# Optimization experiments

Hardware: AMD Instinct MI355X
Metric: run time of the kernel (lower is better)

Reference implementation:

```python
import jax, jax.numpy as jnp
import numpy as np

TOP_K = 30
NUM_RBF = 16
MAX_REL = 32  # max_relative_feature
LN_EPS = 1e-5


def normalize(x, axis=-1, eps=1e-12):
    n = jnp.linalg.norm(x, axis=axis, keepdims=True)
    return x / jnp.maximum(n, eps)


def gather_nodes(nodes, idx):
    # nodes [B,L,C], idx [B,L,K] -> [B,L,K,C]
    B, L, K = idx.shape
    flat = idx.reshape(B, L * K)
    g = jnp.take_along_axis(nodes, flat[:, :, None], axis=1)
    return g.reshape(B, L, K, -1)


def gather_edges(edges, idx):
    # edges [B,L,L,C], idx [B,L,K] -> [B,L,K,C]
    return jnp.take_along_axis(edges, idx[..., None], axis=2)


def _dist(Xca, mask, eps=1e-6):
    mask_2D = mask[:, None, :] * mask[:, :, None]            # [B,L,L]
    dX = Xca[:, None, :, :] - Xca[:, :, None, :]             # [B,L,L,3]
    D = mask_2D * jnp.sqrt(jnp.sum(dX ** 2, -1) + eps)
    D_max = jnp.max(D, -1, keepdims=True)
    D_adjust = D + (1.0 - mask_2D) * D_max
    k = min(TOP_K, Xca.shape[1])
    neg_vals, E_idx = jax.lax.top_k(-D_adjust, k)            # smallest-k
    D_neighbors = -neg_vals
    mask_neighbors = gather_edges(mask_2D[..., None], E_idx)
    return D_neighbors, E_idx, mask_neighbors


def _rbf(D):
    D_mu = jnp.linspace(2.0, 22.0, NUM_RBF)                  # [R]
    D_sigma = (22.0 - 2.0) / NUM_RBF
    return jnp.exp(-(((D[..., None] - D_mu) / D_sigma) ** 2))


def _quaternions(R):
    # R [...,3,3] -> Q [...,4]
    diag = jnp.diagonal(R, axis1=-2, axis2=-1)               # [...,3]
    Rxx, Ryy, Rzz = diag[..., 0], diag[..., 1], diag[..., 2]
    mags = 0.5 * jnp.sqrt(jnp.abs(1 + jnp.stack(
        [Rxx - Ryy - Rzz, -Rxx + Ryy - Rzz, -Rxx - Ryy + Rzz], -1)))
    signs = jnp.sign(jnp.stack([
        R[..., 2, 1] - R[..., 1, 2],
        R[..., 0, 2] - R[..., 2, 0],
        R[..., 1, 0] - R[..., 0, 1]], -1))
    xyz = signs * mags
    w = jnp.sqrt(jax.nn.relu(1 + jnp.sum(diag, -1, keepdims=True))) / 2.0
    return normalize(jnp.concatenate([xyz, w], -1))


def _get_orientations(A, B, C, E_idx, eps=1e-6):
    v1 = A - B
    v2 = C - B
    e1 = v1 / (jnp.linalg.norm(v1, axis=-1, keepdims=True) + eps)
    u2 = v2 - jnp.sum(e1 * v2, -1, keepdims=True) * e1
    e2 = u2 / (jnp.linalg.norm(u2, axis=-1, keepdims=True) + eps)
    e3 = jnp.cross(e1, e2)
    O = jnp.stack([e1, e2, e3], axis=-1)                     # [B,L,3,3] columns
    O9 = O.reshape(O.shape[0], O.shape[1], 9)
    O_nb = gather_nodes(O9, E_idx).reshape(*E_idx.shape, 3, 3)  # [B,L,K,3,3]
    B_nb = gather_nodes(B, E_idx)                            # [B,L,K,3]
    dX = B_nb - B[:, :, None, :]
    dU = normalize(jnp.einsum('blij,blkj->blki', O, dX))
    R = jnp.einsum('blji,blkjm->blkim', O, O_nb)             # O^T @ O_nb
    Q = _quaternions(R)
    return jnp.concatenate([dU, Q], -1)                      # [B,L,K,7]


def _AD_features(Xca, eps=1e-6):
    dX = Xca[:, 1:, :] - Xca[:, :-1, :]
    U = normalize(dX)
    u_2, u_1, u_0 = U[:, :-2], U[:, 1:-1], U[:, 2:]
    n_2 = normalize(jnp.cross(u_2, u_1))
    n_1 = normalize(jnp.cross(u_1, u_0))
    cosA = jnp.clip(-jnp.sum(u_1 * u_0, -1), -1 + eps, 1 - eps)
    A = jnp.arccos(cosA)
    cosD = jnp.clip(jnp.sum(n_2 * n_1, -1), -1 + eps, 1 - eps)
    D = jnp.sign(jnp.sum(u_2 * n_1, -1)) * jnp.arccos(cosD)
    AD = jnp.stack([jnp.cos(A), jnp.sin(A) * jnp.cos(D), jnp.sin(A) * jnp.sin(D)], 2)
    return jnp.pad(AD, ((0, 0), (1, 2), (0, 0)))             # [B,L,3]


def layer_norm(x, g, b):
    mu = jnp.mean(x, -1, keepdims=True)
    var = jnp.var(x, -1, keepdims=True)
    return (x - mu) / jnp.sqrt(var + LN_EPS) * g + b


def setup_inputs() -> dict:
    key = jax.random.key(0)
    ks = jax.random.split(key, 12)
    B, L = 4, 2048
    node_f, edge_f = 128, 128
    edge_in = 16 + NUM_RBF + 7 + 16  # 55 ('coarse')
    s = lambda fan: 1.0 / np.sqrt(fan)
    return {
        'X': jax.random.normal(ks[0], (B, L, 4, 3), jnp.float32),
        'mask': jnp.ones((B, L), jnp.float32),
        'residue_idx': jnp.arange(B * L, dtype=jnp.int32).reshape(B, L),
        'chain_labels': jax.random.randint(ks[1], (B, L), 0, 2, jnp.int32),
        'W_pe': jax.random.uniform(ks[2], (2 * MAX_REL + 1, 16), jnp.float32, -s(65), s(65)),
        'b_pe': jnp.zeros((16,), jnp.float32),
        'W_ch': jax.random.uniform(ks[3], (2, 16), jnp.float32, -s(2), s(2)),
        'b_ch': jnp.zeros((16,), jnp.float32),
        'W_node': jax.random.uniform(ks[4], (3, node_f), jnp.float32, -s(3), s(3)),
        'b_node': jnp.zeros((node_f,), jnp.float32),
        'W_edge': jax.random.uniform(ks[5], (edge_in, edge_f), jnp.float32, -s(edge_in), s(edge_in)),
        'b_edge': jnp.zeros((edge_f,), jnp.float32),
        'g_nodes': jnp.ones((node_f,), jnp.float32),
        'bn_nodes': jnp.zeros((node_f,), jnp.float32),
        'g_edges': jnp.ones((edge_f,), jnp.float32),
        'bn_edges': jnp.zeros((edge_f,), jnp.float32),
    }


def reference(X, mask, residue_idx, chain_labels, W_pe, b_pe, W_ch, b_ch,
              W_node, b_node, W_edge, b_edge, g_nodes, bn_nodes, g_edges, bn_edges):
    N, Ca, C = X[:, :, 0], X[:, :, 1], X[:, :, 2]
    D_neighbors, E_idx, mask_neighbors = _dist(Ca, mask)
    RBF = _rbf(D_neighbors)                                  # [B,L,K,16]
    O_features = _get_orientations(N, Ca, C, E_idx)          # [B,L,K,7]
    # positional encodings from residue-index offsets
    res_nb = jnp.take_along_axis(residue_idx[:, :, None].repeat(E_idx.shape[2], 2) * 0 +
                                 gather_nodes(residue_idx[..., None], E_idx)[..., 0], E_idx * 0, axis=2)
    res_nb = gather_nodes(residue_idx[..., None], E_idx)[..., 0]
    offset = res_nb - residue_idx[:, :, None]
    d = jnp.clip(offset + MAX_REL, 0, 2 * MAX_REL)
    E_positional = W_pe[d] + b_pe                            # [B,L,K,16]
    # chain embedding from same/other-chain indicator
    ch_nb = gather_nodes(chain_labels[..., None], E_idx)[..., 0]
    same = (ch_nb == chain_labels[:, :, None]).astype(jnp.float32)
    E_chains = jnp.stack([same, 1.0 - same], -1) @ W_ch + b_ch  # [B,L,K,16]
    E = jnp.concatenate([E_positional, RBF, O_features, E_chains], -1)
    E = layer_norm(E @ W_edge + b_edge, g_edges, bn_edges)
    V = _AD_features(Ca)                                     # [B,L,3]
    V = layer_norm(V @ W_node + b_node, g_nodes, bn_nodes)
    return V, E, E_idx
```

## Files before the change

kernel.cpp:

```cpp
#include <hip/hip_runtime.h>

#define NB 4
#define NL 2048
#define NK 30
#define NRES (NB*NL)
#define NEDGE (NRES*NK)
#define EPB 64

enum : int {
  WOFF_DNB   = 0,
  WOFF_EIDX  = 245760,
  WOFF_O     = 491520,
  WOFF_WPE   = 565248,
  WOFF_BPE   = 566288,
  WOFF_WCH   = 566304,
  WOFF_BCH   = 566336,
  WOFF_WNODE = 566352,
  WOFF_BNODE = 566736,
  WOFF_WEDGE = 566864,
  WOFF_BEDGE = 573904,
  WOFF_GN    = 574032,
  WOFF_BNN   = 574160,
  WOFF_GE    = 574288,
  WOFF_BNE   = 574416,
  WOFF_PK    = 574544,
};

__device__ __forceinline__ float sgnf(float x) {
  return (x > 0.f) ? 1.f : ((x < 0.f) ? -1.f : 0.f);
}
__device__ __forceinline__ float loadf(const void* p, int idx, bool isbf) {
  if (isbf) return __uint_as_float(((unsigned)((const unsigned short*)p)[idx]) << 16);
  return ((const float*)p)[idx];
}
__device__ __forceinline__ int geti(const void* p, int idx, int mode) {
  if (mode == 0) return ((const int*)p)[idx];
  if (mode == 1) return (int)rintf(((const float*)p)[idx]);
  return (int)rintf(__uint_as_float(((unsigned)((const unsigned short*)p)[idx]) << 16));
}
__device__ __forceinline__ bool probe_bf(const void* maskp) {
  return ((const unsigned*)maskp)[0] == 0x3F803F80u;
}
__device__ __forceinline__ int probe_int(const void* residxp) {
  unsigned w1 = ((const unsigned*)residxp)[1];
  return (w1 == 1u) ? 0 : ((w1 == 0x3F800000u) ? 1 : 2);
}
__device__ __forceinline__ unsigned long long shfl_xor_u64(unsigned long long x, int m) {
  int lo = (int)(unsigned)(x & 0xffffffffull);
  int hi = (int)(unsigned)(x >> 32);
  lo = __shfl_xor(lo, m, 64);
  hi = __shfl_xor(hi, m, 64);
  return ((unsigned long long)(unsigned)hi << 32) | (unsigned)lo;
}

struct ConvArgs {
  const void* src[12];
  int off[12];
  int sz[12];
  const void* maskp;
};

__global__ void prep_kernel(ConvArgs a, float* wsf) {
  const bool isbf = probe_bf(a.maskp);
  const int stride = gridDim.x * blockDim.x;
  const int t0 = blockIdx.x * blockDim.x + threadIdx.x;
  for (int q = 0; q < 12; ++q) {
    float* dst = wsf + a.off[q];
    const int n = a.sz[q];
    for (int i = t0; i < n; i += stride) dst[i] = loadf(a.src[q], i, isbf);
  }
}

__global__ void frames_kernel(const void* Xraw, const void* maskp, float* wsf) {
  const bool isbf = probe_bf(maskp);
  int r = blockIdx.x * blockDim.x + threadIdx.x;
  if (r >= NRES) return;
  const int xb = r * 12;
  float nx = loadf(Xraw, xb+0, isbf), ny = loadf(Xraw, xb+1, isbf), nz = loadf(Xraw, xb+2, isbf);
  float cax= loadf(Xraw, xb+3, isbf), cay= loadf(Xraw, xb+4, isbf), caz= loadf(Xraw, xb+5, isbf);
  float cx = loadf(Xraw, xb+6, isbf), cy = loadf(Xraw, xb+7, isbf), cz = loadf(Xraw, xb+8, isbf);
  float mk = loadf(maskp, r, isbf);
  float4* pko = (float4*)(wsf + WOFF_PK);
  pko[r] = make_float4(cax, cay, caz, mk);
  float v1x=nx-cax, v1y=ny-cay, v1z=nz-caz;
  float v2x=cx-cax, v2y=cy-cay, v2z=cz-caz;
  float n1 = sqrtf(v1x*v1x + v1y*v1y + v1z*v1z) + 1e-6f;
  float e1x=v1x/n1, e1y=v1y/n1, e1z=v1z/n1;
  float dp = e1x*v2x + e1y*v2y + e1z*v2z;
  float u2x=v2x-dp*e1x, u2y=v2y-dp*e1y, u2z=v2z-dp*e1z;
  float n2 = sqrtf(u2x*u2x + u2y*u2y + u2z*u2z) + 1e-6f;
  float e2x=u2x/n2, e2y=u2y/n2, e2z=u2z/n2;
  float e3x = e1y*e2z - e1z*e2y;
  float e3y = e1z*e2x - e1x*e2z;
  float e3z = e1x*e2y - e1y*e2x;
  float* o = wsf + WOFF_O + (size_t)r*9;
  o[0]=e1x; o[1]=e2x; o[2]=e3x;
  o[3]=e1y; o[4]=e2y; o[5]=e3y;
  o[6]=e1z; o[7]=e2z; o[8]=e3z;
}

#define CE(i,j) { unsigned long long a_=q[i], b_=q[j]; bool lt_=a_<b_; \
                  q[i]=lt_?a_:b_; q[j]=lt_?b_:a_; }
#define SORT8(B) CE(B+0,B+1) CE(B+2,B+3) CE(B+4,B+5) CE(B+6,B+7) \
                 CE(B+0,B+2) CE(B+1,B+3) CE(B+4,B+6) CE(B+5,B+7) \
                 CE(B+1,B+2) CE(B+5,B+6) \
                 CE(B+0,B+4) CE(B+1,B+5) CE(B+2,B+6) CE(B+3,B+7) \
                 CE(B+2,B+4) CE(B+3,B+5) \
                 CE(B+1,B+2) CE(B+3,B+4) CE(B+5,B+6)
#define SHIFTQ(B) { q[B+0]=q[B+1]; q[B+1]=q[B+2]; q[B+2]=q[B+3]; q[B+3]=q[B+4]; \
                    q[B+4]=q[B+5]; q[B+5]=q[B+6]; q[B+6]=q[B+7]; q[B+7]=~0ull; }

__global__ __launch_bounds__(256) void topk_kernel(const float* wsf,
                                                   int* eidx, float* dnb,
                                                   float* outf, unsigned long long outEidx) {
#pragma clang fp contract(off)
  const int lane = threadIdx.x & 63;
  const int row = blockIdx.x*4 + (threadIdx.x >> 6);
  const int b = row >> 11, i = row & (NL-1);
  const float4* pb = ((const float4*)(wsf + WOFF_PK)) + b*NL;
  const float4 pi = pb[i];
  const float xi = pi.x, yi = pi.y, zi = pi.z, mi = pi.w;
  unsigned long long q[32];
  float lmax = -1e30f;
  #pragma unroll
  for (int s=0;s<32;s++){
    float4 pj = pb[s*64 + lane];
    float dx=pj.x-xi, dy=pj.y-yi, dz=pj.z-zi;
    float ss = dx*dx;
    ss = ss + dy*dy;
    ss = ss + dz*dz;
    ss = ss + 1e-6f;
    float m2 = mi*pj.w;
    float d = m2 * sqrtf(ss);
    lmax = fmaxf(lmax, d);
    q[s] = ((unsigned long long)__float_as_uint(d) << 32) | (unsigned)(s*64 + lane);
  }
  #pragma unroll
  for (int m=1;m<64;m<<=1) lmax = fmaxf(lmax, __shfl_xor(lmax, m, 64));
  const unsigned dmb = __float_as_uint(lmax);
  #pragma unroll
  for (int s=0;s<32;s++)
    if ((unsigned)(q[s] >> 32) == 0u)
      q[s] = ((unsigned long long)dmb << 32) | (unsigned)q[s];
  SORT8(0) SORT8(8) SORT8(16) SORT8(24)
  const size_t obase = (size_t)row*NK;
  #pragma unroll 1
  for (int k=0;k<NK;k++){
    unsigned long long c01 = q[0]  < q[8]  ? q[0]  : q[8];
    unsigned long long c23 = q[16] < q[24] ? q[16] : q[24];
    unsigned long long cand = c01 < c23 ? c01 : c23;
    float dh = __uint_as_float((unsigned)(cand >> 32));
    float dmin = dh;
    #pragma unroll
    for (int m=1;m<64;m<<=1) dmin = fminf(dmin, __shfl_xor(dmin, m, 64));
    unsigned long long bal = __ballot(dh == dmin);
    unsigned long long best;
    if (__popcll(bal) == 1) {
      int src = __ffsll((long long)bal) - 1;
      int lo = __shfl((int)(unsigned)cand, src, 64);
      best = ((unsigned long long)__float_as_uint(dmin) << 32) | (unsigned)lo;
    } else {
      best = cand;
      #pragma unroll
      for (int m=1;m<64;m<<=1){
        unsigned long long o2 = shfl_xor_u64(best, m);
        best = o2 < best ? o2 : best;
      }
    }
    if (lane==0){
      unsigned j = (unsigned)best;
      eidx[obase + k] = (int)j;
      dnb[obase + k] = __uint_as_float((unsigned)(best >> 32));
      outf[outEidx + obase + k] = (float)j;
    }
    if (cand == best){
      if      (q[0]  == best) SHIFTQ(0)
      else if (q[8]  == best) SHIFTQ(8)
      else if (q[16] == best) SHIFTQ(16)
      else                    SHIFTQ(24)
    }
  }
}

__global__ __launch_bounds__(256) void edge_kernel(const float* wsf, const int* eidx,
                                                   const void* Xraw, const void* maskp,
                                                   const void* residx, const void* chains,
                                                   float* outf, unsigned long long outE) {
  __shared__ float F[55][EPB];
  const bool isbf = probe_bf(maskp);
  const int icmode = probe_int(residx);
  const int t = threadIdx.x;
  const int g = t & 63, sq = t >> 6;
  const int e = blockIdx.x * EPB + g;
  const int row = e / NK;
  const int b = row / NL, i = row % NL;
  const int j = eidx[e];
  const int ri = geti(residx, b*NL + i, icmode), rj = geti(residx, b*NL + j, icmode);
  int dd = rj - ri + 32;
  dd = dd < 0 ? 0 : (dd > 64 ? 64 : dd);
  const int ci = geti(chains, b*NL + i, icmode), cj = geti(chains, b*NL + j, icmode);
  const float D = wsf[WOFF_DNB + e];
  #pragma unroll
  for (int u = 0; u < 4; ++u) {
    const int s = sq*4 + u;
    F[s][g] = wsf[WOFF_WPE + dd*16 + s] + wsf[WOFF_BPE + s];
    float mu = (float)(2.0 + s * (20.0 / 15.0));
    float tt = (D - mu) / 1.25f;
    F[16+s][g] = expf(-(tt*tt));
    float w = (ci == cj) ? wsf[WOFF_WCH + s] : wsf[WOFF_WCH + 16 + s];
    F[39+s][g] = w + wsf[WOFF_BCH + s];
  }
  if (g < 16) {
    const int gq = sq*16 + g;
    const int eq = blockIdx.x * EPB + gq;
    const int rowq = eq / NK;
    const int bq = rowq / NL;
    const int jq = eidx[eq];
    const float* Oi = wsf + WOFF_O + (size_t)rowq*9;
    const float* Oj = wsf + WOFF_O + ((size_t)(bq*NL + jq))*9;
    const int ci_ = rowq*12 + 3, cj_ = (bq*NL + jq)*12 + 3;
    float dx = loadf(Xraw, cj_+0, isbf) - loadf(Xraw, ci_+0, isbf);
    float dy = loadf(Xraw, cj_+1, isbf) - loadf(Xraw, ci_+1, isbf);
    float dz = loadf(Xraw, cj_+2, isbf) - loadf(Xraw, ci_+2, isbf);
    float du0 = Oi[0]*dx + Oi[1]*dy + Oi[2]*dz;
    float du1 = Oi[3]*dx + Oi[4]*dy + Oi[5]*dz;
    float du2 = Oi[6]*dx + Oi[7]*dy + Oi[8]*dz;
    float n = fmaxf(sqrtf(du0*du0 + du1*du1 + du2*du2), 1e-12f);
    F[32][gq] = du0/n; F[33][gq] = du1/n; F[34][gq] = du2/n;
    float R[3][3];
    #pragma unroll
    for (int a2=0;a2<3;a2++)
      #pragma unroll
      for (int m=0;m<3;m++)
        R[a2][m] = Oi[0*3+a2]*Oj[0*3+m] + Oi[1*3+a2]*Oj[1*3+m] + Oi[2*3+a2]*Oj[2*3+m];
    float mx = 0.5f*sqrtf(fabsf(1.0f + R[0][0] - R[1][1] - R[2][2]));
    float my = 0.5f*sqrtf(fabsf(1.0f - R[0][0] + R[1][1] - R[2][2]));
    float mz = 0.5f*sqrtf(fabsf(1.0f - R[0][0] - R[1][1] + R[2][2]));
    float qx = sgnf(R[2][1]-R[1][2]) * mx;
    float qy = sgnf(R[0][2]-R[2][0]) * my;
    float qz = sgnf(R[1][0]-R[0][1]) * mz;
    float qw = sqrtf(fmaxf(1.0f + R[0][0] + R[1][1] + R[2][2], 0.0f)) / 2.0f;
    float qn = fmaxf(sqrtf(qx*qx + qy*qy + qz*qz + qw*qw), 1e-12f);
    F[35][gq] = qx/qn; F[36][gq] = qy/qn; F[37][gq] = qz/qn; F[38][gq] = qw/qn;
  }
  __syncthreads();
  const int wv = t >> 6, lane = t & 63;
  const int eg = lane >> 4;
  const int cg = lane & 15;
  const int ebase = wv*16 + eg*4;
  const int c0 = cg*8;
  const float4* W4 = (const float4*)(wsf + WOFF_WEDGE);
  const float4 beA = *(const float4*)(wsf + WOFF_BEDGE + c0);
  const float4 beB = *(const float4*)(wsf + WOFF_BEDGE + c0 + 4);
  float acc[4][8];
  #pragma unroll
  for (int qq=0;qq<4;qq++){
    acc[qq][0]=beA.x; acc[qq][1]=beA.y; acc[qq][2]=beA.z; acc[qq][3]=beA.w;
    acc[qq][4]=beB.x; acc[qq][5]=beB.y; acc[qq][6]=beB.z; acc[qq][7]=beB.w;
  }
  for (int d = 0; d < 55; ++d) {
    float4 f  = *(const float4*)&F[d][ebase];
    float4 wa = W4[d*32 + cg*2];
    float4 wb = W4[d*32 + cg*2 + 1];
    #pragma unroll
    for (int qq=0;qq<4;qq++){
      float fq = (qq==0)?f.x:(qq==1)?f.y:(qq==2)?f.z:f.w;
      acc[qq][0] = fmaf(fq, wa.x, acc[qq][0]);
      acc[qq][1] = fmaf(fq, wa.y, acc[qq][1]);
      acc[qq][2] = fmaf(fq, wa.z, acc[qq][2]);
      acc[qq][3] = fmaf(fq, wa.w, acc[qq][3]);
      acc[qq][4] = fmaf(fq, wb.x, acc[qq][4]);
      acc[qq][5] = fmaf(fq, wb.y, acc[qq][5]);
      acc[qq][6] = fmaf(fq, wb.z, acc[qq][6]);
      acc[qq][7] = fmaf(fq, wb.w, acc[qq][7]);
    }
  }
  const float4 geA = *(const float4*)(wsf + WOFF_GE + c0);
  const float4 geB = *(const float4*)(wsf + WOFF_GE + c0 + 4);
  const float4 bnA = *(const float4*)(wsf + WOFF_BNE + c0);
  const float4 bnB = *(const float4*)(wsf + WOFF_BNE + c0 + 4);
  #pragma unroll
  for (int qq=0;qq<4;qq++){
    float s = ((acc[qq][0]+acc[qq][1])+(acc[qq][2]+acc[qq][3]))
            + ((acc[qq][4]+acc[qq][5])+(acc[qq][6]+acc[qq][7]));
    s += __shfl_xor(s, 1, 64); s += __shfl_xor(s, 2, 64);
    s += __shfl_xor(s, 4, 64); s += __shfl_xor(s, 8, 64);
    float mu_ = s * (1.0f/128.0f);
    float dv[8];
    #pragma unroll
    for (int jj=0;jj<8;jj++) dv[jj] = acc[qq][jj] - mu_;
    float v = ((dv[0]*dv[0]+dv[1]*dv[1])+(dv[2]*dv[2]+dv[3]*dv[3]))
            + ((dv[4]*dv[4]+dv[5]*dv[5])+(dv[6]*dv[6]+dv[7]*dv[7]));
    v += __shfl_xor(v, 1, 64); v += __shfl_xor(v, 2, 64);
    v += __shfl_xor(v, 4, 64); v += __shfl_xor(v, 8, 64);
    float inv = 1.0f / sqrtf(v * (1.0f/128.0f) + 1e-5f);
    float4 oA, oB;
    oA.x = dv[0]*inv*geA.x + bnA.x; oA.y = dv[1]*inv*geA.y + bnA.y;
    oA.z = dv[2]*inv*geA.z + bnA.z; oA.w = dv[3]*inv*geA.w + bnA.w;
    oB.x = dv[4]*inv*geB.x + bnB.x; oB.y = dv[5]*inv*geB.y + bnB.y;
    oB.z = dv[6]*inv*geB.z + bnB.z; oB.w = dv[7]*inv*geB.w + bnB.w;
    float* op = outf + outE + (size_t)(blockIdx.x*EPB + ebase + qq)*128 + c0;
    *(float4*)op       = oA;
    *(float4*)(op + 4) = oB;
  }
}

__global__ __launch_bounds__(256) void node_kernel(const float* wsf, const void* Xraw,
                                                   const void* maskp, float* outf) {
  const bool isbf = probe_bf(maskp);
  const int gw = (blockIdx.x * 256 + threadIdx.x) >> 6;
  const int lane = threadIdx.x & 63;
  const int b = gw / NL, l = gw % NL;
  float ad0 = 0.f, ad1 = 0.f, ad2 = 0.f;
  if (l >= 1 && l <= NL - 3) {
    const int base = (b*NL)*12;
    float p0x = loadf(Xraw, base+(l-1)*12+3, isbf), p0y = loadf(Xraw, base+(l-1)*12+4, isbf), p0z = loadf(Xraw, base+(l-1)*12+5, isbf);
    float p1x = loadf(Xraw, base+(l  )*12+3, isbf), p1y = loadf(Xraw, base+(l  )*12+4, isbf), p1z = loadf(Xraw, base+(l  )*12+5, isbf);
    float p2x = loadf(Xraw, base+(l+1)*12+3, isbf), p2y = loadf(Xraw, base+(l+1)*12+4, isbf), p2z = loadf(Xraw, base+(l+1)*12+5, isbf);
    float p3x = loadf(Xraw, base+(l+2)*12+3, isbf), p3y = loadf(Xraw, base+(l+2)*12+4, isbf), p3z = loadf(Xraw, base+(l+2)*12+5, isbf);
    float u2x=p1x-p0x, u2y=p1y-p0y, u2z=p1z-p0z;
    float u1x=p2x-p1x, u1y=p2y-p1y, u1z=p2z-p1z;
    float u0x=p3x-p2x, u0y=p3y-p2y, u0z=p3z-p2z;
    float nn;
    nn = fmaxf(sqrtf(u2x*u2x+u2y*u2y+u2z*u2z), 1e-12f); u2x/=nn; u2y/=nn; u2z/=nn;
    nn = fmaxf(sqrtf(u1x*u1x+u1y*u1y+u1z*u1z), 1e-12f); u1x/=nn; u1y/=nn; u1z/=nn;
    nn = fmaxf(sqrtf(u0x*u0x+u0y*u0y+u0z*u0z), 1e-12f); u0x/=nn; u0y/=nn; u0z/=nn;
    float n2x = u2y*u1z - u2z*u1y, n2y = u2z*u1x - u2x*u1z, n2z = u2x*u1y - u2y*u1x;
    float n1x = u1y*u0z - u1z*u0y, n1y = u1z*u0x - u1x*u0z, n1z = u1x*u0y - u1y*u0x;
    nn = fmaxf(sqrtf(n2x*n2x+n2y*n2y+n2z*n2z), 1e-12f); n2x/=nn; n2y/=nn; n2z/=nn;
    nn = fmaxf(sqrtf(n1x*n1x+n1y*n1y+n1z*n1z), 1e-12f); n1x/=nn; n1y/=nn; n1z/=nn;
    const float lo = (float)(-1.0 + 1e-6), hi = (float)(1.0 - 1e-6);
    float cosA = -(u1x*u0x + u1y*u0y + u1z*u0z);
    cosA = fminf(fmaxf(cosA, lo), hi);
    float A = acosf(cosA);
    float cosD = n2x*n1x + n2y*n1y + n2z*n1z;
    cosD = fminf(fmaxf(cosD, lo), hi);
    float Dd = sgnf(u2x*n1x + u2y*n1y + u2z*n1z) * acosf(cosD);
    ad0 = cosf(A);
    ad1 = sinf(A) * cosf(Dd);
    ad2 = sinf(A) * sinf(Dd);
  }
  const int c0 = 2*lane, c1 = c0 + 1;
  float acc0 = wsf[WOFF_BNODE+c0] + ad0*wsf[WOFF_WNODE+c0] + ad1*wsf[WOFF_WNODE+128+c0] + ad2*wsf[WOFF_WNODE+256+c0];
  float acc1 = wsf[WOFF_BNODE+c1] + ad0*wsf[WOFF_WNODE+c1] + ad1*wsf[WOFF_WNODE+128+c1] + ad2*wsf[WOFF_WNODE+256+c1];
  float s = acc0 + acc1;
  for (int m=1;m<64;m<<=1) s += __shfl_xor(s, m, 64);
  float mu_ = s * (1.0f/128.0f);
  float d0 = acc0 - mu_, d1 = acc1 - mu_;
  float v = d0*d0 + d1*d1;
  for (int m=1;m<64;m<<=1) v += __shfl_xor(v, m, 64);
  float inv = 1.0f / sqrtf(v * (1.0f/128.0f) + 1e-5f);
  float y0 = d0*inv*wsf[WOFF_GN + c0] + wsf[WOFF_BNN + c0];
  float y1 = d1*inv*wsf[WOFF_GN + c1] + wsf[WOFF_BNN + c1];
  float2 pk; pk.x = y0; pk.y = y1;
  *((float2*)(outf + (size_t)gw*128 + c0)) = pk;
}

extern "C" void kernel_launch(void* const* d_in, const int* in_sizes, int n_in,
                              void* d_out, int out_size, void* d_ws, size_t ws_size,
                              hipStream_t stream) {
  float* wsf = (float*)d_ws;
  int* eidx = (int*)(wsf + WOFF_EIDX);
  float* dnb = wsf + WOFF_DNB;
  float* outf = (float*)d_out;
  const void* Xraw = d_in[0];
  const void* maskp = d_in[1];

  unsigned long long outEidx = (unsigned long long)out_size - NEDGE;
  unsigned long long outE    = outEidx - (unsigned long long)NEDGE*128;

  ConvArgs ca;
  const int fsz[12]  = {1040, 16, 32, 16, 384, 128, 7040, 128, 128, 128, 128, 128};
  const int foff[12] = {WOFF_WPE, WOFF_BPE, WOFF_WCH, WOFF_BCH, WOFF_WNODE, WOFF_BNODE,
                        WOFF_WEDGE, WOFF_BEDGE, WOFF_GN, WOFF_BNN, WOFF_GE, WOFF_BNE};
  for (int q = 0; q < 12; ++q) { ca.src[q] = d_in[4 + q]; ca.off[q] = foff[q]; ca.sz[q] = fsz[q]; }
  ca.maskp = maskp;

  prep_kernel<<<40, 256, 0, stream>>>(ca, wsf);
  frames_kernel<<<NRES/256, 256, 0, stream>>>(Xraw, maskp, wsf);
  topk_kernel<<<NRES/4, 256, 0, stream>>>(wsf, eidx, dnb, outf, outEidx);
  edge_kernel<<<NEDGE/EPB, 256, 0, stream>>>(wsf, eidx, Xraw, maskp, d_in[2], d_in[3], outf, outE);
  node_kernel<<<NRES/4, 256, 0, stream>>>(wsf, Xraw, maskp, outf);
}
```

Baseline: 306.4 us.

## Merge prep/frames and topk/node kernels; double edges per block in edge kernel

Folds the weight-conversion and frame computation into one launch split by block index. It also merges the top-k and node-feature kernels into a single launch with disjoint block ranges, which cuts launch overhead and lets the independent node work overlap with top-k. The edge kernel now handles 128 edges per block, with 8 edges per thread in the projection loop for more weight reuse, and all 128 threads compute orientation features directly. The cost is higher register pressure from the 8x8 accumulator and twice the shared memory.

```diff
diff --git a/kernel.cpp b/kernel.cpp
--- a/kernel.cpp
+++ b/kernel.cpp
@@ -5,7 +5,7 @@
 #define NK 30
 #define NRES (NB*NL)
 #define NEDGE (NRES*NK)
-#define EPB 64
+#define EPB 128
 
 enum : int {
   WOFF_DNB   = 0,
@@ -60,43 +60,42 @@
   const void* maskp;
 };
 
-__global__ void prep_kernel(ConvArgs a, float* wsf) {
+__global__ void pf_kernel(ConvArgs a, const void* Xraw, float* wsf) {
   const bool isbf = probe_bf(a.maskp);
-  const int stride = gridDim.x * blockDim.x;
-  const int t0 = blockIdx.x * blockDim.x + threadIdx.x;
-  for (int q = 0; q < 12; ++q) {
-    float* dst = wsf + a.off[q];
-    const int n = a.sz[q];
-    for (int i = t0; i < n; i += stride) dst[i] = loadf(a.src[q], i, isbf);
-  }
-}
-
-__global__ void frames_kernel(const void* Xraw, const void* maskp, float* wsf) {
-  const bool isbf = probe_bf(maskp);
-  int r = blockIdx.x * blockDim.x + threadIdx.x;
-  if (r >= NRES) return;
-  const int xb = r * 12;
-  float nx = loadf(Xraw, xb+0, isbf), ny = loadf(Xraw, xb+1, isbf), nz = loadf(Xraw, xb+2, isbf);
-  float cax= loadf(Xraw, xb+3, isbf), cay= loadf(Xraw, xb+4, isbf), caz= loadf(Xraw, xb+5, isbf);
-  float cx = loadf(Xraw, xb+6, isbf), cy = loadf(Xraw, xb+7, isbf), cz = loadf(Xraw, xb+8, isbf);
-  float mk = loadf(maskp, r, isbf);
-  float4* pko = (float4*)(wsf + WOFF_PK);
-  pko[r] = make_float4(cax, cay, caz, mk);
-  float v1x=nx-cax, v1y=ny-cay, v1z=nz-caz;
-  float v2x=cx-cax, v2y=cy-cay, v2z=cz-caz;
-  float n1 = sqrtf(v1x*v1x + v1y*v1y + v1z*v1z) + 1e-6f;
-  float e1x=v1x/n1, e1y=v1y/n1, e1z=v1z/n1;
-  float dp = e1x*v2x + e1y*v2y + e1z*v2z;
-  float u2x=v2x-dp*e1x, u2y=v2y-dp*e1y, u2z=v2z-dp*e1z;
-  float n2 = sqrtf(u2x*u2x + u2y*u2y + u2z*u2z) + 1e-6f;
-  float e2x=u2x/n2, e2y=u2y/n2, e2z=u2z/n2;
-  float e3x = e1y*e2z - e1z*e2y;
-  float e3y = e1z*e2x - e1x*e2z;
-  float e3z = e1x*e2y - e1y*e2x;
-  float* o = wsf + WOFF_O + (size_t)r*9;
-  o[0]=e1x; o[1]=e2x; o[2]=e3x;
-  o[3]=e1y; o[4]=e2y; o[5]=e3y;
-  o[6]=e1z; o[7]=e2z; o[8]=e3z;
+  const int t = threadIdx.x;
+  if (blockIdx.x < 32) {
+    const int r = blockIdx.x * 256 + t;
+    const int xb = r * 12;
+    float nx = loadf(Xraw, xb+0, isbf), ny = loadf(Xraw, xb+1, isbf), nz = loadf(Xraw, xb+2, isbf);
+    float cax= loadf(Xraw, xb+3, isbf), cay= loadf(Xraw, xb+4, isbf), caz= loadf(Xraw, xb+5, isbf);
+    float cx = loadf(Xraw, xb+6, isbf), cy = loadf(Xraw, xb+7, isbf), cz = loadf(Xraw, xb+8, isbf);
+    float mk = loadf(a.maskp, r, isbf);
+    float4* pko = (float4*)(wsf + WOFF_PK);
+    pko[r] = make_float4(cax, cay, caz, mk);
+    float v1x=nx-cax, v1y=ny-cay, v1z=nz-caz;
+    float v2x=cx-cax, v2y=cy-cay, v2z=cz-caz;
+    float n1 = sqrtf(v1x*v1x + v1y*v1y + v1z*v1z) + 1e-6f;
+    float e1x=v1x/n1, e1y=v1y/n1, e1z=v1z/n1;
+    float dp = e1x*v2x + e1y*v2y + e1z*v2z;
+    float u2x=v2x-dp*e1x, u2y=v2y-dp*e1y, u2z=v2z-dp*e1z;
+    float n2 = sqrtf(u2x*u2x + u2y*u2y + u2z*u2z) + 1e-6f;
+    float e2x=u2x/n2, e2y=u2y/n2, e2z=u2z/n2;
+    float e3x = e1y*e2z - e1z*e2y;
+    float e3y = e1z*e2x - e1x*e2z;
+    float e3z = e1x*e2y - e1y*e2x;
+    float* o = wsf + WOFF_O + (size_t)r*9;
+    o[0]=e1x; o[1]=e2x; o[2]=e3x;
+    o[3]=e1y; o[4]=e2y; o[5]=e3y;
+    o[6]=e1z; o[7]=e2z; o[8]=e3z;
+  } else {
+    const int stride = 40 * 256;
+    const int t0 = (blockIdx.x - 32) * 256 + t;
+    for (int q = 0; q < 12; ++q) {
+      float* dst = wsf + a.off[q];
+      const int n = a.sz[q];
+      for (int i = t0; i < n; i += stride) dst[i] = loadf(a.src[q], i, isbf);
+    }
+  }
 }
 
 #define CE(i,j) { unsigned long long a_=q[i], b_=q[j]; bool lt_=a_<b_; \
@@ -110,12 +109,11 @@
 #define SHIFTQ(B) { q[B+0]=q[B+1]; q[B+1]=q[B+2]; q[B+2]=q[B+3]; q[B+3]=q[B+4]; \
                     q[B+4]=q[B+5]; q[B+5]=q[B+6]; q[B+6]=q[B+7]; q[B+7]=~0ull; }
 
-__global__ __launch_bounds__(256) void topk_kernel(const float* wsf,
-                                                   int* eidx, float* dnb,
-                                                   float* outf, unsigned long long outEidx) {
+__device__ __forceinline__ void topk_body(int blk, const float* wsf, int* eidx, float* dnb,
+                                          float* outf, unsigned long long outEidx) {
 #pragma clang fp contract(off)
   const int lane = threadIdx.x & 63;
-  const int row = blockIdx.x*4 + (threadIdx.x >> 6);
+  const int row = blk*4 + (threadIdx.x >> 6);
   const int b = row >> 11, i = row & (NL-1);
   const float4* pb = ((const float4*)(wsf + WOFF_PK)) + b*NL;
   const float4 pi = pb[i];
@@ -182,133 +180,10 @@
   }
 }
 
-__global__ __launch_bounds__(256) void edge_kernel(const float* wsf, const int* eidx,
-                                                   const void* Xraw, const void* maskp,
-                                                   const void* residx, const void* chains,
-                                                   float* outf, unsigned long long outE) {
-  __shared__ float F[55][EPB];
+__device__ __forceinline__ void node_body(int blk, const float* wsf, const void* Xraw,
+                                          const void* maskp, float* outf) {
   const bool isbf = probe_bf(maskp);
-  const int icmode = probe_int(residx);
-  const int t = threadIdx.x;
-  const int g = t & 63, sq = t >> 6;
-  const int e = blockIdx.x * EPB + g;
-  const int row = e / NK;
-  const int b = row / NL, i = row % NL;
-  const int j = eidx[e];
-  const int ri = geti(residx, b*NL + i, icmode), rj = geti(residx, b*NL + j, icmode);
-  int dd = rj - ri + 32;
-  dd = dd < 0 ? 0 : (dd > 64 ? 64 : dd);
-  const int ci = geti(chains, b*NL + i, icmode), cj = geti(chains, b*NL + j, icmode);
-  const float D = wsf[WOFF_DNB + e];
-  #pragma unroll
-  for (int u = 0; u < 4; ++u) {
-    const int s = sq*4 + u;
-    F[s][g] = wsf[WOFF_WPE + dd*16 + s] + wsf[WOFF_BPE + s];
-    float mu = (float)(2.0 + s * (20.0 / 15.0));
-    float tt = (D - mu) / 1.25f;
-    F[16+s][g] = expf(-(tt*tt));
-    float w = (ci == cj) ? wsf[WOFF_WCH + s] : wsf[WOFF_WCH + 16 + s];
-    F[39+s][g] = w + wsf[WOFF_BCH + s];
-  }
-  if (g < 16) {
-    const int gq = sq*16 + g;
-    const int eq = blockIdx.x * EPB + gq;
-    const int rowq = eq / NK;
-    const int bq = rowq / NL;
-    const int jq = eidx[eq];
-    const float* Oi = wsf + WOFF_O + (size_t)rowq*9;
-    const float* Oj = wsf + WOFF_O + ((size_t)(bq*NL + jq))*9;
-    const int ci_ = rowq*12 + 3, cj_ = (bq*NL + jq)*12 + 3;
-    float dx = loadf(Xraw, cj_+0, isbf) - loadf(Xraw, ci_+0, isbf);
-    float dy = loadf(Xraw, cj_+1, isbf) - loadf(Xraw, ci_+1, isbf);
-    float dz = loadf(Xraw, cj_+2, isbf) - loadf(Xraw, ci_+2, isbf);
-    float du0 = Oi[0]*dx + Oi[1]*dy + Oi[2]*dz;
-    float du1 = Oi[3]*dx + Oi[4]*dy + Oi[5]*dz;
-    float du2 = Oi[6]*dx + Oi[7]*dy + Oi[8]*dz;
-    float n = fmaxf(sqrtf(du0*du0 + du1*du1 + du2*du2), 1e-12f);
-    F[32][gq] = du0/n; F[33][gq] = du1/n; F[34][gq] = du2/n;
-    float R[3][3];
-    #pragma unroll
-    for (int a2=0;a2<3;a2++)
-      #pragma unroll
-      for (int m=0;m<3;m++)
-        R[a2][m] = Oi[0*3+a2]*Oj[0*3+m] + Oi[1*3+a2]*Oj[1*3+m] + Oi[2*3+a2]*Oj[2*3+m];
-    float mx = 0.5f*sqrtf(fabsf(1.0f + R[0][0] - R[1][1] - R[2][2]));
-    float my = 0.5f*sqrtf(fabsf(1.0f - R[0][0] + R[1][1] - R[2][2]));
-    float mz = 0.5f*sqrtf(fabsf(1.0f - R[0][0] - R[1][1] + R[2][2]));
-    float qx = sgnf(R[2][1]-R[1][2]) * mx;
-    float qy = sgnf(R[0][2]-R[2][0]) * my;
-    float qz = sgnf(R[1][0]-R[0][1]) * mz;
-    float qw = sqrtf(fmaxf(1.0f + R[0][0] + R[1][1] + R[2][2], 0.0f)) / 2.0f;
-    float qn = fmaxf(sqrtf(qx*qx + qy*qy + qz*qz + qw*qw), 1e-12f);
-    F[35][gq] = qx/qn; F[36][gq] = qy/qn; F[37][gq] = qz/qn; F[38][gq] = qw/qn;
-  }
-  __syncthreads();
-  const int wv = t >> 6, lane = t & 63;
-  const int eg = lane >> 4;
-  const int cg = lane & 15;
-  const int ebase = wv*16 + eg*4;
-  const int c0 = cg*8;
-  const float4* W4 = (const float4*)(wsf + WOFF_WEDGE);
-  const float4 beA = *(const float4*)(wsf + WOFF_BEDGE + c0);
-  const float4 beB = *(const float4*)(wsf + WOFF_BEDGE + c0 + 4);
-  float acc[4][8];
-  #pragma unroll
-  for (int qq=0;qq<4;qq++){
-    acc[qq][0]=beA.x; acc[qq][1]=beA.y; acc[qq][2]=beA.z; acc[qq][3]=beA.w;
-    acc[qq][4]=beB.x; acc[qq][5]=beB.y; acc[qq][6]=beB.z; acc[qq][7]=beB.w;
-  }
-  for (int d = 0; d < 55; ++d) {
-    float4 f  = *(const float4*)&F[d][ebase];
-    float4 wa = W4[d*32 + cg*2];
-    float4 wb = W4[d*32 + cg*2 + 1];
-    #pragma unroll
-    for (int qq=0;qq<4;qq++){
-      float fq = (qq==0)?f.x:(qq==1)?f.y:(qq==2)?f.z:f.w;
-      acc[qq][0] = fmaf(fq, wa.x, acc[qq][0]);
-      acc[qq][1] = fmaf(fq, wa.y, acc[qq][1]);
-      acc[qq][2] = fmaf(fq, wa.z, acc[qq][2]);
-      acc[qq][3] = fmaf(fq, wa.w, acc[qq][3]);
-      acc[qq][4] = fmaf(fq, wb.x, acc[qq][4]);
-      acc[qq][5] = fmaf(fq, wb.y, acc[qq][5]);
-      acc[qq][6] = fmaf(fq, wb.z, acc[qq][6]);
-      acc[qq][7] = fmaf(fq, wb.w, acc[qq][7]);
-    }
-  }
-  const float4 geA = *(const float4*)(wsf + WOFF_GE + c0);
-  const float4 geB = *(const float4*)(wsf + WOFF_GE + c0 + 4);
-  const float4 bnA = *(const float4*)(wsf + WOFF_BNE + c0);
-  const float4 bnB = *(const float4*)(wsf + WOFF_BNE + c0 + 4);
-  #pragma unroll
-  for (int qq=0;qq<4;qq++){
-    float s = ((acc[qq][0]+acc[qq][1])+(acc[qq][2]+acc[qq][3]))
-            + ((acc[qq][4]+acc[qq][5])+(acc[qq][6]+acc[qq][7]));
-    s += __shfl_xor(s, 1, 64); s += __shfl_xor(s, 2, 64);
-    s += __shfl_xor(s, 4, 64); s += __shfl_xor(s, 8, 64);
-    float mu_ = s * (1.0f/128.0f);
-    float dv[8];
-    #pragma unroll
-    for (int jj=0;jj<8;jj++) dv[jj] = acc[qq][jj] - mu_;
-    float v = ((dv[0]*dv[0]+dv[1]*dv[1])+(dv[2]*dv[2]+dv[3]*dv[3]))
-            + ((dv[4]*dv[4]+dv[5]*dv[5])+(dv[6]*dv[6]+dv[7]*dv[7]));
-    v += __shfl_xor(v, 1, 64); v += __shfl_xor(v, 2, 64);
-    v += __shfl_xor(v, 4, 64); v += __shfl_xor(v, 8, 64);
-    float inv = 1.0f / sqrtf(v * (1.0f/128.0f) + 1e-5f);
-    float4 oA, oB;
-    oA.x = dv[0]*inv*geA.x + bnA.x; oA.y = dv[1]*inv*geA.y + bnA.y;
-    oA.z = dv[2]*inv*geA.z + bnA.z; oA.w = dv[3]*inv*geA.w + bnA.w;
-    oB.x = dv[4]*inv*geB.x + bnB.x; oB.y = dv[5]*inv*geB.y + bnB.y;
-    oB.z = dv[6]*inv*geB.z + bnB.z; oB.w = dv[7]*inv*geB.w + bnB.w;
-    float* op = outf + outE + (size_t)(blockIdx.x*EPB + ebase + qq)*128 + c0;
-    *(float4*)op       = oA;
-    *(float4*)(op + 4) = oB;
-  }
-}
-
-__global__ __launch_bounds__(256) void node_kernel(const float* wsf, const void* Xraw,
-                                                   const void* maskp, float* outf) {
-  const bool isbf = probe_bf(maskp);
-  const int gw = (blockIdx.x * 256 + threadIdx.x) >> 6;
+  const int gw = (blk * 256 + (int)threadIdx.x) >> 6;
   const int lane = threadIdx.x & 63;
   const int b = gw / NL, l = gw % NL;
   float ad0 = 0.f, ad1 = 0.f, ad2 = 0.f;
@@ -356,6 +231,133 @@
   *((float2*)(outf + (size_t)gw*128 + c0)) = pk;
 }
 
+__global__ __launch_bounds__(256) void tn_kernel(const float* wsf, int* eidx, float* dnb,
+                                                 float* outf, unsigned long long outEidx,
+                                                 const void* Xraw, const void* maskp) {
+  if (blockIdx.x < NRES/4) topk_body(blockIdx.x, wsf, eidx, dnb, outf, outEidx);
+  else                     node_body(blockIdx.x - NRES/4, wsf, Xraw, maskp, outf);
+}
+
+__global__ __launch_bounds__(256) void edge_kernel(const float* wsf, const int* eidx,
+                                                   const void* Xraw, const void* maskp,
+                                                   const void* residx, const void* chains,
+                                                   float* outf, unsigned long long outE) {
+  __shared__ float F[55][EPB];
+  const bool isbf = probe_bf(maskp);
+  const int icmode = probe_int(residx);
+  const int t = threadIdx.x;
+  const int g = t & 127, h = t >> 7;
+  const int e = blockIdx.x * EPB + g;
+  const int row = e / NK;
+  const int b = row / NL, i = row % NL;
+  const int j = eidx[e];
+  const int ri = geti(residx, b*NL + i, icmode), rj = geti(residx, b*NL + j, icmode);
+  int dd = rj - ri + 32;
+  dd = dd < 0 ? 0 : (dd > 64 ? 64 : dd);
+  const int ci = geti(chains, b*NL + i, icmode), cj = geti(chains, b*NL + j, icmode);
+  const float D = wsf[WOFF_DNB + e];
+  #pragma unroll
+  for (int u = 0; u < 8; ++u) {
+    const int s = h*8 + u;
+    F[s][g] = wsf[WOFF_WPE + dd*16 + s] + wsf[WOFF_BPE + s];
+    float mu = (float)(2.0 + s * (20.0 / 15.0));
+    float tt = (D - mu) / 1.25f;
+    F[16+s][g] = expf(-(tt*tt));
+    float w = (ci == cj) ? wsf[WOFF_WCH + s] : wsf[WOFF_WCH + 16 + s];
+    F[39+s][g] = w + wsf[WOFF_BCH + s];
+  }
+  if (t < 128) {
+    const float* Oi = wsf + WOFF_O + (size_t)row*9;
+    const float* Oj = wsf + WOFF_O + ((size_t)(b*NL + j))*9;
+    const int ci_ = row*12 + 3, cj_ = (b*NL + j)*12 + 3;
+    float dx = loadf(Xraw, cj_+0, isbf) - loadf(Xraw, ci_+0, isbf);
+    float dy = loadf(Xraw, cj_+1, isbf) - loadf(Xraw, ci_+1, isbf);
+    float dz = loadf(Xraw, cj_+2, isbf) - loadf(Xraw, ci_+2, isbf);
+    float du0 = Oi[0]*dx + Oi[1]*dy + Oi[2]*dz;
+    float du1 = Oi[3]*dx + Oi[4]*dy + Oi[5]*dz;
+    float du2 = Oi[6]*dx + Oi[7]*dy + Oi[8]*dz;
+    float n = fmaxf(sqrtf(du0*du0 + du1*du1 + du2*du2), 1e-12f);
+    F[32][g] = du0/n; F[33][g] = du1/n; F[34][g] = du2/n;
+    float R[3][3];
+    #pragma unroll
+    for (int a2=0;a2<3;a2++)
+      #pragma unroll
+      for (int m=0;m<3;m++)
+        R[a2][m] = Oi[0*3+a2]*Oj[0*3+m] + Oi[1*3+a2]*Oj[1*3+m] + Oi[2*3+a2]*Oj[2*3+m];
+    float mx = 0.5f*sqrtf(fabsf(1.0f + R[0][0] - R[1][1] - R[2][2]));
+    float my = 0.5f*sqrtf(fabsf(1.0f - R[0][0] + R[1][1] - R[2][2]));
+    float mz = 0.5f*sqrtf(fabsf(1.0f - R[0][0] - R[1][1] + R[2][2]));
+    float qx = sgnf(R[2][1]-R[1][2]) * mx;
+    float qy = sgnf(R[0][2]-R[2][0]) * my;
+    float qz = sgnf(R[1][0]-R[0][1]) * mz;
+    float qw = sqrtf(fmaxf(1.0f + R[0][0] + R[1][1] + R[2][2], 0.0f)) / 2.0f;
+    float qn = fmaxf(sqrtf(qx*qx + qy*qy + qz*qz + qw*qw), 1e-12f);
+    F[35][g] = qx/qn; F[36][g] = qy/qn; F[37][g] = qz/qn; F[38][g] = qw/qn;
+  }
+  __syncthreads();
+  const int wv = t >> 6, lane = t & 63;
+  const int eg = lane >> 4;
+  const int cg = lane & 15;
+  const int ebase = wv*32 + eg*8;
+  const int c0 = cg*8;
+  const float4* W4 = (const float4*)(wsf + WOFF_WEDGE);
+  const float4 beA = *(const float4*)(wsf + WOFF_BEDGE + c0);
+  const float4 beB = *(const float4*)(wsf + WOFF_BEDGE + c0 + 4);
+  float acc[8][8];
+  #pragma unroll
+  for (int qq=0;qq<8;qq++){
+    acc[qq][0]=beA.x; acc[qq][1]=beA.y; acc[qq][2]=beA.z; acc[qq][3]=beA.w;
+    acc[qq][4]=beB.x; acc[qq][5]=beB.y; acc[qq][6]=beB.z; acc[qq][7]=beB.w;
+  }
+  for (int d = 0; d < 55; ++d) {
+    float4 f0 = *(const float4*)&F[d][ebase];
+    float4 f1 = *(const float4*)&F[d][ebase+4];
+    float4 wa = W4[d*32 + cg*2];
+    float4 wb = W4[d*32 + cg*2 + 1];
+    #pragma unroll
+    for (int qq=0;qq<8;qq++){
+      float fq = (qq==0)?f0.x:(qq==1)?f0.y:(qq==2)?f0.z:(qq==3)?f0.w:
+                 (qq==4)?f1.x:(qq==5)?f1.y:(qq==6)?f1.z:f1.w;
+      acc[qq][0] = fmaf(fq, wa.x, acc[qq][0]);
+      acc[qq][1] = fmaf(fq, wa.y, acc[qq][1]);
+      acc[qq][2] = fmaf(fq, wa.z, acc[qq][2]);
+      acc[qq][3] = fmaf(fq, wa.w, acc[qq][3]);
+      acc[qq][4] = fmaf(fq, wb.x, acc[qq][4]);
+      acc[qq][5] = fmaf(fq, wb.y, acc[qq][5]);
+      acc[qq][6] = fmaf(fq, wb.z, acc[qq][6]);
+      acc[qq][7] = fmaf(fq, wb.w, acc[qq][7]);
+    }
+  }
+  const float4 geA = *(const float4*)(wsf + WOFF_GE + c0);
+  const float4 geB = *(const float4*)(wsf + WOFF_GE + c0 + 4);
+  const float4 bnA = *(const float4*)(wsf + WOFF_BNE + c0);
+  const float4 bnB = *(const float4*)(wsf + WOFF_BNE + c0 + 4);
+  #pragma unroll
+  for (int qq=0;qq<8;qq++){
+    float s = ((acc[qq][0]+acc[qq][1])+(acc[qq][2]+acc[qq][3]))
+            + ((acc[qq][4]+acc[qq][5])+(acc[qq][6]+acc[qq][7]));
+    s += __shfl_xor(s, 1, 64); s += __shfl_xor(s, 2, 64);
+    s += __shfl_xor(s, 4, 64); s += __shfl_xor(s, 8, 64);
+    float mu_ = s * (1.0f/128.0f);
+    float dv[8];
+    #pragma unroll
+    for (int jj=0;jj<8;jj++) dv[jj] = acc[qq][jj] - mu_;
+    float v = ((dv[0]*dv[0]+dv[1]*dv[1])+(dv[2]*dv[2]+dv[3]*dv[3]))
+            + ((dv[4]*dv[4]+dv[5]*dv[5])+(dv[6]*dv[6]+dv[7]*dv[7]));
+    v += __shfl_xor(v, 1, 64); v += __shfl_xor(v, 2, 64);
+    v += __shfl_xor(v, 4, 64); v += __shfl_xor(v, 8, 64);
+    float inv = 1.0f / sqrtf(v * (1.0f/128.0f) + 1e-5f);
+    float4 oA, oB;
+    oA.x = dv[0]*inv*geA.x + bnA.x; oA.y = dv[1]*inv*geA.y + bnA.y;
+    oA.z = dv[2]*inv*geA.z + bnA.z; oA.w = dv[3]*inv*geA.w + bnA.w;
+    oB.x = dv[4]*inv*geB.x + bnB.x; oB.y = dv[5]*inv*geB.y + bnB.y;
+    oB.z = dv[6]*inv*geB.z + bnB.z; oB.w = dv[7]*inv*geB.w + bnB.w;
+    float* op = outf + outE + (size_t)(blockIdx.x*EPB + ebase + qq)*128 + c0;
+    *(float4*)op       = oA;
+    *(float4*)(op + 4) = oB;
+  }
+}
+
 extern "C" void kernel_launch(void* const* d_in, const int* in_sizes, int n_in,
                               void* d_out, int out_size, void* d_ws, size_t ws_size,
                               hipStream_t stream) {
@@ -376,9 +378,7 @@
   for (int q = 0; q < 12; ++q) { ca.src[q] = d_in[4 + q]; ca.off[q] = foff[q]; ca.sz[q] = fsz[q]; }
   ca.maskp = maskp;
 
-  prep_kernel<<<40, 256, 0, stream>>>(ca, wsf);
-  frames_kernel<<<NRES/256, 256, 0, stream>>>(Xraw, maskp, wsf);
-  topk_kernel<<<NRES/4, 256, 0, stream>>>(wsf, eidx, dnb, outf, outEidx);
+  pf_kernel<<<72, 256, 0, stream>>>(ca, Xraw, wsf);
+  tn_kernel<<<NRES/4 + NRES/4, 256, 0, stream>>>(wsf, eidx, dnb, outf, outEidx, Xraw, maskp);
   edge_kernel<<<NEDGE/EPB, 256, 0, stream>>>(wsf, eidx, Xraw, maskp, d_in[2], d_in[3], outf, outE);
-  node_kernel<<<NRES/4, 256, 0, stream>>>(wsf, Xraw, maskp, outf);
-}
+}
```

Result: no change. 309.4 us (+1.0%).
